# Performance work log

Measured on AMD Instinct MI355X. Metric: run time of the kernel, lower is better.

The kernel has to match this reference:

```python
import jax, jax.numpy as jnp
import numpy as np

B, F, O, DEG = 8192, 512, 512, 15  # degree+1 = 16 basis terms


def setup_inputs() -> dict:
    key = jax.random.key(0)
    k1, k2, k3 = jax.random.split(key, 3)
    x = jax.random.normal(k1, (B, F), dtype=jnp.float32)
    coeffs = jax.random.normal(k2, (F, O, DEG + 1), dtype=jnp.float32) * 0.05
    base_weight = jax.random.normal(k3, (F, O), dtype=jnp.float32) * 0.05
    return {"x": x, "coeffs": coeffs, "base_weight": base_weight}


def _chebyshev_basis(x, degree):
    # x: [B, F] -> basis: [B, F, degree+1], vectorized across all features.
    t = jnp.tanh(x)
    T0 = jnp.ones_like(t)
    T1 = t
    basis = [T0, T1]
    for _ in range(2, degree + 1):
        basis.append(2.0 * t * basis[-1] - basis[-2])
    return jnp.stack(basis, axis=-1)  # [B, F, D+1]


def reference(x, coeffs, base_weight):
    basis = _chebyshev_basis(x, DEG)                      # [B, F, D+1]
    poly_out = jnp.einsum('bin,ion->bo', basis, coeffs)   # [B, O]
    kl = jnp.zeros((1,), dtype=x.dtype)
    residual = x @ base_weight                            # [B, O]
    return (poly_out + residual, kl)
```

## Files before the change

### kernel.cpp

```cpp
#include <hip/hip_runtime.h>
#include <hip/hip_bf16.h>
#include <stdint.h>

#define MB_ 8192
#define FD  512
#define OD  512
#define KD  8704
#define KBASIS 8192
#define BT_KS   1088
#define BT_CHUNKS_PER_CT (BT_KS * 128)
#define BT_BYTES_PER_CT  (BT_CHUNKS_PER_CT * 16)
#define TOFF 98304

typedef __attribute__((ext_vector_type(4))) float f32x4;
typedef __attribute__((ext_vector_type(8))) short bf16x8;
typedef __attribute__((ext_vector_type(4))) unsigned int u32x4;
typedef __attribute__((ext_vector_type(2))) unsigned int u32x2;

__device__ __forceinline__ void gload_lds16(const void* g, void* l) {
  __builtin_amdgcn_global_load_lds((const __attribute__((address_space(1))) void*)g,
                                   (__attribute__((address_space(3))) void*)l,
                                   16, 0, 0);
}

__device__ __forceinline__ uint32_t bf_rtn(float f) {
  uint32_t u = __float_as_uint(f);
  return (u + 0x7fffu + ((u >> 16) & 1u)) >> 16;
}

__device__ __forceinline__ uint32_t pk(float a, float b) {
  uint32_t r;
  asm("v_cvt_pk_bf16_f32 %0, %1, %2" : "=v"(r) : "v"(a), "v"(b));
  return r;
}

__global__ __launch_bounds__(256) void k_tanh(const float* __restrict__ x,
                                              float* __restrict__ t,
                                              uint16_t* __restrict__ xbf) {
  int i = blockIdx.x * 256 + threadIdx.x;
  f32x4 v = ((const f32x4*)x)[i];
  f32x4 tv;
  tv[0] = tanhf(v[0]); tv[1] = tanhf(v[1]);
  tv[2] = tanhf(v[2]); tv[3] = tanhf(v[3]);
  ((f32x4*)t)[i] = tv;
  u32x2 p;
  p[0] = pk(v[0], v[1]);
  p[1] = pk(v[2], v[3]);
  ((u32x2*)xbf)[i] = p;
}

__global__ __launch_bounds__(256) void k_bt(const float* __restrict__ coeffs,
                                            const float* __restrict__ bw,
                                            uint16_t* __restrict__ bt2,
                                            float* __restrict__ out) {
  int tid = blockIdx.x * 256 + threadIdx.x;
  {
    int o = tid & 511, i = tid >> 9;
    const f32x4* src = (const f32x4*)(coeffs + (((size_t)(i * 512 + o)) << 4));
    f32x4 c0 = src[0], c1 = src[1], c2 = src[2], c3 = src[3];
    u32x4 qa, qb;
    qa[0] = pk(c0[0], c0[1]);
    qa[1] = pk(c0[2], c0[3]);
    qa[2] = pk(c1[0], c1[1]);
    qa[3] = pk(c1[2], c1[3]);
    qb[0] = pk(c2[0], c2[1]);
    qb[1] = pk(c2[2], c2[3]);
    qb[2] = pk(c3[0], c3[1]);
    qb[3] = pk(c3[2], c3[3]);
    int slo = ((i >> 2) << 3) | (i & 3);
    size_t cidx = (size_t)(o >> 7) * BT_CHUNKS_PER_CT + (size_t)slo * 128 + (o & 127);
    u32x4* base = (u32x4*)bt2;
    base[cidx]       = qa;
    base[cidx + 512] = qb;
  }
  {
    int o2 = tid >> 9, i2 = tid & 511;
    size_t cidx = (size_t)(o2 >> 7) * BT_CHUNKS_PER_CT + (size_t)(1024 + (i2 >> 3)) * 128 + (o2 & 127);
    bt2[cidx * 8 + (i2 & 7)] = (uint16_t)bf_rtn(bw[i2 * 512 + o2]);
  }
  if (tid == 0) out[(size_t)MB_ * OD] = 0.0f;
}

__global__ __launch_bounds__(512, 2) void k_gemm(const float* __restrict__ t,
                                                 const uint16_t* __restrict__ xbf,
                                                 const uint16_t* __restrict__ bt2,
                                                 float* __restrict__ out) {
  __shared__ __align__(128) char lds[110592];

  const int tid  = threadIdx.x;
  const int lane = tid & 63;
  const int wid  = tid >> 6;
  const int wr   = wid >> 1;
  const int wc   = wid & 1;
  const int l15  = lane & 15, l4 = lane >> 4;

  int bx  = blockIdx.x;
  int idx = bx >> 3;
  int rt  = (bx & 7) * 8 + (idx >> 2);
  int ct  = idx & 3;
  const int brow = rt << 7, bcol = ct << 7;

  const char* btbase = (const char*)bt2 + (size_t)ct * BT_BYTES_PER_CT;
  const int row = brow + wr * 32 + l15;
  const uint16_t* x0 = xbf + (size_t)row * FD;
  const uint16_t* x1 = x0 + (size_t)16 * FD;

  const char* bb0 = lds + l4 * 2048 + (wc * 64 + l15) * 16;
  const char* tb0 = lds + TOFF + (wr * 32 + l15) * 16 + l4 * 4;
  char* sBl = lds + tid * 16;
  char* sTl = lds + TOFF + wid * 1024 + lane * 16;

  const char* sBgBase = btbase + (size_t)tid * 16;
  const char* sTgBase = (const char*)t + (((size_t)(brow + wid * 64 + lane)) * FD) * 4;

  f32x4 acc[2][4];
#pragma unroll
  for (int m = 0; m < 2; ++m)
#pragma unroll
    for (int n = 0; n < 4; ++n) acc[m][n] = (f32x4)0.0f;

  u32x4 pf00 = {}, pf01 = {}, pf10 = {}, pf11 = {};

  auto stageB = [&](int s2, int b2) {
    const char* src = sBgBase + ((size_t)s2 << 14);
    gload_lds16(src, sBl + b2 * 16384);
    gload_lds16(src + 8192, sBl + b2 * 16384 + 8192);
  };
  auto stageT = [&](int s2, int b2) {
    if (wid < 2)
      gload_lds16(sTgBase + ((size_t)s2 << 4), sTl + b2 * 2048);
  };
  auto chains = [&](const char* tb, u32x4& af00, u32x4& af01,
                    u32x4& af10, u32x4& af11) {
#pragma unroll
    for (int m = 0; m < 2; ++m) {
      float tv = *(const float*)(tb + m * 256);
      float c2 = tv + tv;
      float T0 = 1.0f, T1 = tv;
      float T2  = __builtin_fmaf(c2, T1,  -T0);
      float T3  = __builtin_fmaf(c2, T2,  -T1);
      float T4  = __builtin_fmaf(c2, T3,  -T2);
      float T5  = __builtin_fmaf(c2, T4,  -T3);
      float T6  = __builtin_fmaf(c2, T5,  -T4);
      float T7  = __builtin_fmaf(c2, T6,  -T5);
      float T8  = __builtin_fmaf(c2, T7,  -T6);
      float T9  = __builtin_fmaf(c2, T8,  -T7);
      float T10 = __builtin_fmaf(c2, T9,  -T8);
      float T11 = __builtin_fmaf(c2, T10, -T9);
      float T12 = __builtin_fmaf(c2, T11, -T10);
      float T13 = __builtin_fmaf(c2, T12, -T11);
      float T14 = __builtin_fmaf(c2, T13, -T12);
      float T15 = __builtin_fmaf(c2, T14, -T13);
      u32x4 lo, hi;
      lo[0] = pk(T0,  T1);  lo[1] = pk(T2,  T3);
      lo[2] = pk(T4,  T5);  lo[3] = pk(T6,  T7);
      hi[0] = pk(T8,  T9);  hi[1] = pk(T10, T11);
      hi[2] = pk(T12, T13); hi[3] = pk(T14, T15);
      if (m == 0) { af00 = lo; af01 = hi; }
      else        { af10 = lo; af11 = hi; }
    }
  };
  auto mfma16 = [&](const char* bb, const u32x4& af00, const u32x4& af01,
                    const u32x4& af10, const u32x4& af11) {
    bf16x8 a00 = *(const bf16x8*)&af00;
    bf16x8 a01 = *(const bf16x8*)&af01;
    bf16x8 a10 = *(const bf16x8*)&af10;
    bf16x8 a11 = *(const bf16x8*)&af11;
#pragma unroll
    for (int n = 0; n < 4; ++n) {
      bf16x8 b0 = *(const bf16x8*)(bb + n * 256);
      bf16x8 b1 = *(const bf16x8*)(bb + 8192 + n * 256);
      acc[0][n] = __builtin_amdgcn_mfma_f32_16x16x32_bf16(a00, b0, acc[0][n], 0, 0, 0);
      acc[1][n] = __builtin_amdgcn_mfma_f32_16x16x32_bf16(a10, b0, acc[1][n], 0, 0, 0);
      acc[0][n] = __builtin_amdgcn_mfma_f32_16x16x32_bf16(a01, b1, acc[0][n], 0, 0, 0);
      acc[1][n] = __builtin_amdgcn_mfma_f32_16x16x32_bf16(a11, b1, acc[1][n], 0, 0, 0);
    }
  };
  auto fence_bar = [&]() {
    if (wid < 2) asm volatile("s_waitcnt vmcnt(6)" ::: "memory");
    else         asm volatile("s_waitcnt vmcnt(4)" ::: "memory");
    __builtin_amdgcn_s_barrier();
    asm volatile("" ::: "memory");
  };

  stageB(0, 0); stageT(0, 0);
  stageB(1, 1); stageT(1, 1);
  stageB(2, 2); stageT(2, 2);
  stageB(3, 3); stageT(3, 3);
  fence_bar();

  auto pairbody = [&](int s, int c0, int c1, int g0, int g1) {
    stageB(s + 4, g0); stageT(s + 4, g0);
    stageB(s + 5, g1); stageT(s + 5, g1);
    u32x4 af00, af01, af10, af11;
    chains(tb0 + c0 * 2048, af00, af01, af10, af11);
    __builtin_amdgcn_s_setprio(1);
    mfma16(bb0 + c0 * 16384, af00, af01, af10, af11);
    __builtin_amdgcn_s_setprio(0);
    chains(tb0 + c1 * 2048, af00, af01, af10, af11);
    __builtin_amdgcn_s_setprio(1);
    mfma16(bb0 + c1 * 16384, af00, af01, af10, af11);
    __builtin_amdgcn_s_setprio(0);
    fence_bar();
  };

  for (int s = 0; s < 120; s += 6) {
    pairbody(s,     0, 1, 4, 5);
    pairbody(s + 2, 2, 3, 0, 1);
    pairbody(s + 4, 4, 5, 2, 3);
  }
  pairbody(120, 0, 1, 4, 5);
  pairbody(122, 2, 3, 0, 1);

  for (int s = 124; s < 136; ++s) {
    u32x4 af00 = pf00, af01 = pf01, af10 = pf10, af11 = pf11;
    if (s >= 126 && s <= 133) stageB(s + 2, (s + 2) % 6);
    if (s >= 127 && s <= 134) {
      int kres = ((s + 1 - 128) << 6) + l4 * 8;
      pf00 = *(const u32x4*)(x0 + kres);
      pf01 = *(const u32x4*)(x0 + kres + 32);
      pf10 = *(const u32x4*)(x1 + kres);
      pf11 = *(const u32x4*)(x1 + kres + 32);
    }
    if (s < 128)
      chains(tb0 + (s % 6) * 2048, af00, af01, af10, af11);
    mfma16(bb0 + (s % 6) * 16384, af00, af01, af10, af11);
    __syncthreads();
  }

#pragma unroll
  for (int m = 0; m < 2; ++m)
#pragma unroll
    for (int n = 0; n < 4; ++n)
#pragma unroll
      for (int r = 0; r < 4; ++r) {
        int grow = brow + wr * 32 + m * 16 + l4 * 4 + r;
        int gcol = bcol + wc * 64 + n * 16 + l15;
        out[(size_t)grow * OD + gcol] = acc[m][n][r];
      }
}

extern "C" void kernel_launch(void* const* d_in, const int* in_sizes, int n_in,
                              void* d_out, int out_size, void* d_ws, size_t ws_size,
                              hipStream_t stream) {
  const float* x      = (const float*)d_in[0];
  const float* coeffs = (const float*)d_in[1];
  const float* bw     = (const float*)d_in[2];
  float* out = (float*)d_out;
  char* ws = (char*)d_ws;

  float*    t   = (float*)ws;
  uint16_t* xbf = (uint16_t*)(ws + (size_t)16777216);
  uint16_t* bt2 = (uint16_t*)(ws + (size_t)16777216 + 8388608);

  k_tanh<<<4096, 256, 0, stream>>>(x, t, xbf);
  k_bt<<<1024, 256, 0, stream>>>(coeffs, bw, bt2, out);
  k_gemm<<<256, 512, 0, stream>>>(t, xbf, bt2, out);
}
```

Measured before the change: 104.2 us.

## Halve GEMM column tile to 64 and double grid with smaller LDS footprint

Shrinks the output tile of the fused Chebyshev GEMM from 128x128 to 128x64, so 512 workgroups launch instead of 256. The B staging buffer halves, LDS drops to about 60KB and launch bounds target 4 blocks per CU, all meant to raise occupancy and fill the 256 CUs better. The fine-grained vmcnt fences are replaced by plain __syncthreads. In exchange, each block recomputes the Chebyshev basis chains for half as many outputs, which doubles the chain work and the T loads per unit of MFMA work. A-operand reuse also drops.

```diff
diff --git a/kernel.cpp b/kernel.cpp
--- a/kernel.cpp
+++ b/kernel.cpp
@@ -10,7 +10,7 @@
 #define BT_KS   1088
 #define BT_CHUNKS_PER_CT (BT_KS * 128)
 #define BT_BYTES_PER_CT  (BT_CHUNKS_PER_CT * 16)
-#define TOFF 98304
+#define TOFF 49152
 
 typedef __attribute__((ext_vector_type(4))) float f32x4;
 typedef __attribute__((ext_vector_type(8))) short bf16x8;
@@ -81,11 +81,11 @@
   if (tid == 0) out[(size_t)MB_ * OD] = 0.0f;
 }
 
-__global__ __launch_bounds__(512, 2) void k_gemm(const float* __restrict__ t,
+__global__ __launch_bounds__(512, 4) void k_gemm(const float* __restrict__ t,
                                                  const uint16_t* __restrict__ xbf,
                                                  const uint16_t* __restrict__ bt2,
                                                  float* __restrict__ out) {
-  __shared__ __align__(128) char lds[110592];
+  __shared__ __align__(128) char lds[61440];
 
   const int tid  = threadIdx.x;
   const int lane = tid & 63;
@@ -96,35 +96,34 @@
 
   int bx  = blockIdx.x;
   int idx = bx >> 3;
-  int rt  = (bx & 7) * 8 + (idx >> 2);
-  int ct  = idx & 3;
-  const int brow = rt << 7, bcol = ct << 7;
-
-  const char* btbase = (const char*)bt2 + (size_t)ct * BT_BYTES_PER_CT;
+  int rt  = (bx & 7) * 8 + (idx >> 3);
+  int ct  = idx & 7;
+  const int brow = rt << 7, bcol = ct << 6;
+
+  const char* btbase = (const char*)bt2 + (size_t)(ct >> 1) * BT_BYTES_PER_CT;
+  const int colOff = (ct & 1) * 1024;
   const int row = brow + wr * 32 + l15;
   const uint16_t* x0 = xbf + (size_t)row * FD;
   const uint16_t* x1 = x0 + (size_t)16 * FD;
 
-  const char* bb0 = lds + l4 * 2048 + (wc * 64 + l15) * 16;
+  const char* bb0 = lds + l4 * 1024 + (wc * 32 + l15) * 16;
   const char* tb0 = lds + TOFF + (wr * 32 + l15) * 16 + l4 * 4;
   char* sBl = lds + tid * 16;
   char* sTl = lds + TOFF + wid * 1024 + lane * 16;
 
-  const char* sBgBase = btbase + (size_t)tid * 16;
+  const char* sBgBase = btbase + (size_t)wid * 2048 + colOff + (size_t)lane * 16;
   const char* sTgBase = (const char*)t + (((size_t)(brow + wid * 64 + lane)) * FD) * 4;
 
-  f32x4 acc[2][4];
+  f32x4 acc[2][2];
 #pragma unroll
   for (int m = 0; m < 2; ++m)
 #pragma unroll
-    for (int n = 0; n < 4; ++n) acc[m][n] = (f32x4)0.0f;
+    for (int n = 0; n < 2; ++n) acc[m][n] = (f32x4)0.0f;
 
   u32x4 pf00 = {}, pf01 = {}, pf10 = {}, pf11 = {};
 
   auto stageB = [&](int s2, int b2) {
-    const char* src = sBgBase + ((size_t)s2 << 14);
-    gload_lds16(src, sBl + b2 * 16384);
-    gload_lds16(src + 8192, sBl + b2 * 16384 + 8192);
+    gload_lds16(sBgBase + ((size_t)s2 << 14), sBl + b2 * 8192);
   };
   auto stageT = [&](int s2, int b2) {
     if (wid < 2)
@@ -160,34 +159,31 @@
       else        { af10 = lo; af11 = hi; }
     }
   };
-  auto mfma16 = [&](const char* bb, const u32x4& af00, const u32x4& af01,
-                    const u32x4& af10, const u32x4& af11) {
+  auto mfma8 = [&](const char* bb, const u32x4& af00, const u32x4& af01,
+                   const u32x4& af10, const u32x4& af11) {
     bf16x8 a00 = *(const bf16x8*)&af00;
     bf16x8 a01 = *(const bf16x8*)&af01;
     bf16x8 a10 = *(const bf16x8*)&af10;
     bf16x8 a11 = *(const bf16x8*)&af11;
-#pragma unroll
-    for (int n = 0; n < 4; ++n) {
-      bf16x8 b0 = *(const bf16x8*)(bb + n * 256);
-      bf16x8 b1 = *(const bf16x8*)(bb + 8192 + n * 256);
-      acc[0][n] = __builtin_amdgcn_mfma_f32_16x16x32_bf16(a00, b0, acc[0][n], 0, 0, 0);
-      acc[1][n] = __builtin_amdgcn_mfma_f32_16x16x32_bf16(a10, b0, acc[1][n], 0, 0, 0);
-      acc[0][n] = __builtin_amdgcn_mfma_f32_16x16x32_bf16(a01, b1, acc[0][n], 0, 0, 0);
-      acc[1][n] = __builtin_amdgcn_mfma_f32_16x16x32_bf16(a11, b1, acc[1][n], 0, 0, 0);
-    }
-  };
-  auto fence_bar = [&]() {
-    if (wid < 2) asm volatile("s_waitcnt vmcnt(6)" ::: "memory");
-    else         asm volatile("s_waitcnt vmcnt(4)" ::: "memory");
-    __builtin_amdgcn_s_barrier();
-    asm volatile("" ::: "memory");
+    bf16x8 b00 = *(const bf16x8*)(bb);
+    bf16x8 b01 = *(const bf16x8*)(bb + 256);
+    bf16x8 b10 = *(const bf16x8*)(bb + 4096);
+    bf16x8 b11 = *(const bf16x8*)(bb + 4096 + 256);
+    acc[0][0] = __builtin_amdgcn_mfma_f32_16x16x32_bf16(a00, b00, acc[0][0], 0, 0, 0);
+    acc[0][1] = __builtin_amdgcn_mfma_f32_16x16x32_bf16(a00, b01, acc[0][1], 0, 0, 0);
+    acc[1][0] = __builtin_amdgcn_mfma_f32_16x16x32_bf16(a10, b00, acc[1][0], 0, 0, 0);
+    acc[1][1] = __builtin_amdgcn_mfma_f32_16x16x32_bf16(a10, b01, acc[1][1], 0, 0, 0);
+    acc[0][0] = __builtin_amdgcn_mfma_f32_16x16x32_bf16(a01, b10, acc[0][0], 0, 0, 0);
+    acc[0][1] = __builtin_amdgcn_mfma_f32_16x16x32_bf16(a01, b11, acc[0][1], 0, 0, 0);
+    acc[1][0] = __builtin_amdgcn_mfma_f32_16x16x32_bf16(a11, b10, acc[1][0], 0, 0, 0);
+    acc[1][1] = __builtin_amdgcn_mfma_f32_16x16x32_bf16(a11, b11, acc[1][1], 0, 0, 0);
   };
 
   stageB(0, 0); stageT(0, 0);
   stageB(1, 1); stageT(1, 1);
   stageB(2, 2); stageT(2, 2);
   stageB(3, 3); stageT(3, 3);
-  fence_bar();
+  __syncthreads();
 
   auto pairbody = [&](int s, int c0, int c1, int g0, int g1) {
     stageB(s + 4, g0); stageT(s + 4, g0);
@@ -195,13 +191,13 @@
     u32x4 af00, af01, af10, af11;
     chains(tb0 + c0 * 2048, af00, af01, af10, af11);
     __builtin_amdgcn_s_setprio(1);
-    mfma16(bb0 + c0 * 16384, af00, af01, af10, af11);
+    mfma8(bb0 + c0 * 8192, af00, af01, af10, af11);
     __builtin_amdgcn_s_setprio(0);
     chains(tb0 + c1 * 2048, af00, af01, af10, af11);
     __builtin_amdgcn_s_setprio(1);
-    mfma16(bb0 + c1 * 16384, af00, af01, af10, af11);
+    mfma8(bb0 + c1 * 8192, af00, af01, af10, af11);
     __builtin_amdgcn_s_setprio(0);
-    fence_bar();
+    __syncthreads();
   };
 
   for (int s = 0; s < 120; s += 6) {
@@ -224,18 +220,18 @@
     }
     if (s < 128)
       chains(tb0 + (s % 6) * 2048, af00, af01, af10, af11);
-    mfma16(bb0 + (s % 6) * 16384, af00, af01, af10, af11);
+    mfma8(bb0 + (s % 6) * 8192, af00, af01, af10, af11);
     __syncthreads();
   }
 
 #pragma unroll
   for (int m = 0; m < 2; ++m)
 #pragma unroll
-    for (int n = 0; n < 4; ++n)
+    for (int n = 0; n < 2; ++n)
 #pragma unroll
       for (int r = 0; r < 4; ++r) {
         int grow = brow + wr * 32 + m * 16 + l4 * 4 + r;
-        int gcol = bcol + wc * 64 + n * 16 + l15;
+        int gcol = bcol + wc * 32 + n * 16 + l15;
         out[(size_t)grow * OD + gcol] = acc[m][n][r];
       }
 }
@@ -255,5 +251,5 @@
 
   k_tanh<<<4096, 256, 0, stream>>>(x, t, xbf);
   k_bt<<<1024, 256, 0, stream>>>(coeffs, bw, bt2, out);
-  k_gemm<<<256, 512, 0, stream>>>(t, xbf, bt2, out);
-}
+  k_gemm<<<512, 512, 0, stream>>>(t, xbf, bt2, out);
+}
```

After: 114.7 us. 10.0% more time.

## Split GEMM K dimension across two block sets with partial-sum add kernel

Applied to the files above, without the earlier changes.

The fused Chebyshev/residual GEMM is split along K into two halves. 256 blocks handle the basis terms for the first half of the features and write to the output, while another 256 blocks handle the rest plus the residual x·W part and write to a workspace buffer. A separate kernel then adds the two partials. The LDS pipeline is cut from 6 to 4 stages to shrink shared memory for 4 blocks per CU, and stage refills are moved after a barrier. The aim is to fill more of the machine (512 blocks instead of 256), at the cost of an extra 16 MB partial write/read and another launch, with a fallback when the workspace is too small.

```diff
diff --git a/kernel.cpp b/kernel.cpp
--- a/kernel.cpp
+++ b/kernel.cpp
@@ -10,7 +10,12 @@
 #define BT_KS   1088
 #define BT_CHUNKS_PER_CT (BT_KS * 128)
 #define BT_BYTES_PER_CT  (BT_CHUNKS_PER_CT * 16)
-#define TOFF 98304
+#define TOFF 65536
+#define WS_T    16777216ull
+#define WS_XBF  8388608ull
+#define WS_BT2  8912896ull
+#define WS_P1_OFF (WS_T + WS_XBF + WS_BT2)
+#define WS_NEED   (WS_P1_OFF + 16777216ull)
 
 typedef __attribute__((ext_vector_type(4))) float f32x4;
 typedef __attribute__((ext_vector_type(8))) short bf16x8;
@@ -81,11 +86,13 @@
   if (tid == 0) out[(size_t)MB_ * OD] = 0.0f;
 }
 
-__global__ __launch_bounds__(512, 2) void k_gemm(const float* __restrict__ t,
-                                                 const uint16_t* __restrict__ xbf,
-                                                 const uint16_t* __restrict__ bt2,
-                                                 float* __restrict__ out) {
-  __shared__ __align__(128) char lds[110592];
+template <int MODE>
+__device__ __forceinline__ void gemm_body(int bx, char* lds,
+                                          const float* __restrict__ t,
+                                          const uint16_t* __restrict__ xbf,
+                                          const uint16_t* __restrict__ bt2,
+                                          float* __restrict__ outp) {
+  constexpr int S0 = (MODE == 2) ? 68 : 0;
 
   const int tid  = threadIdx.x;
   const int lane = tid & 63;
@@ -94,7 +101,6 @@
   const int wc   = wid & 1;
   const int l15  = lane & 15, l4 = lane >> 4;
 
-  int bx  = blockIdx.x;
   int idx = bx >> 3;
   int rt  = (bx & 7) * 8 + (idx >> 2);
   int ct  = idx & 3;
@@ -121,14 +127,14 @@
 
   u32x4 pf00 = {}, pf01 = {}, pf10 = {}, pf11 = {};
 
-  auto stageB = [&](int s2, int b2) {
-    const char* src = sBgBase + ((size_t)s2 << 14);
+  auto stageB = [&](int gs, int b2) {
+    const char* src = sBgBase + ((size_t)gs << 14);
     gload_lds16(src, sBl + b2 * 16384);
     gload_lds16(src + 8192, sBl + b2 * 16384 + 8192);
   };
-  auto stageT = [&](int s2, int b2) {
+  auto stageT = [&](int gs, int b2) {
     if (wid < 2)
-      gload_lds16(sTgBase + ((size_t)s2 << 4), sTl + b2 * 2048);
+      gload_lds16(sTgBase + ((size_t)gs << 4), sTl + b2 * 2048);
   };
   auto chains = [&](const char* tb, u32x4& af00, u32x4& af01,
                     u32x4& af10, u32x4& af11) {
@@ -180,18 +186,9 @@
     if (wid < 2) asm volatile("s_waitcnt vmcnt(6)" ::: "memory");
     else         asm volatile("s_waitcnt vmcnt(4)" ::: "memory");
     __builtin_amdgcn_s_barrier();
-    asm volatile("" ::: "memory");
-  };
-
-  stageB(0, 0); stageT(0, 0);
-  stageB(1, 1); stageT(1, 1);
-  stageB(2, 2); stageT(2, 2);
-  stageB(3, 3); stageT(3, 3);
-  fence_bar();
-
-  auto pairbody = [&](int s, int c0, int c1, int g0, int g1) {
-    stageB(s + 4, g0); stageT(s + 4, g0);
-    stageB(s + 5, g1); stageT(s + 5, g1);
+    __builtin_amdgcn_sched_barrier(0);
+  };
+  auto pairbody = [&](int s, int c0, int c1) {
     u32x4 af00, af01, af10, af11;
     chains(tb0 + c0 * 2048, af00, af01, af10, af11);
     __builtin_amdgcn_s_setprio(1);
@@ -201,31 +198,60 @@
     __builtin_amdgcn_s_setprio(1);
     mfma16(bb0 + c1 * 16384, af00, af01, af10, af11);
     __builtin_amdgcn_s_setprio(0);
+    __builtin_amdgcn_s_barrier();
+    __builtin_amdgcn_sched_barrier(0);
+    stageB(S0 + s + 4, c0); stageT(S0 + s + 4, c0);
+    stageB(S0 + s + 5, c1); stageT(S0 + s + 5, c1);
     fence_bar();
   };
 
-  for (int s = 0; s < 120; s += 6) {
-    pairbody(s,     0, 1, 4, 5);
-    pairbody(s + 2, 2, 3, 0, 1);
-    pairbody(s + 4, 4, 5, 2, 3);
-  }
-  pairbody(120, 0, 1, 4, 5);
-  pairbody(122, 2, 3, 0, 1);
-
-  for (int s = 124; s < 136; ++s) {
-    u32x4 af00 = pf00, af01 = pf01, af10 = pf10, af11 = pf11;
-    if (s >= 126 && s <= 133) stageB(s + 2, (s + 2) % 6);
-    if (s >= 127 && s <= 134) {
-      int kres = ((s + 1 - 128) << 6) + l4 * 8;
-      pf00 = *(const u32x4*)(x0 + kres);
-      pf01 = *(const u32x4*)(x0 + kres + 32);
-      pf10 = *(const u32x4*)(x1 + kres);
-      pf11 = *(const u32x4*)(x1 + kres + 32);
-    }
-    if (s < 128)
-      chains(tb0 + (s % 6) * 2048, af00, af01, af10, af11);
-    mfma16(bb0 + (s % 6) * 16384, af00, af01, af10, af11);
-    __syncthreads();
+  stageB(S0 + 0, 0); stageT(S0 + 0, 0);
+  stageB(S0 + 1, 1); stageT(S0 + 1, 1);
+  stageB(S0 + 2, 2); stageT(S0 + 2, 2);
+  stageB(S0 + 3, 3); stageT(S0 + 3, 3);
+  fence_bar();
+
+  if constexpr (MODE == 0) {
+    for (int s = 0; s < 120; s += 4) { pairbody(s, 0, 1); pairbody(s + 2, 2, 3); }
+    pairbody(120, 0, 1); pairbody(122, 2, 3);
+    for (int s = 124; s < 136; ++s) {
+      u32x4 af00 = pf00, af01 = pf01, af10 = pf10, af11 = pf11;
+      if (s >= 126 && s <= 133) stageB(s + 2, (s + 2) & 3);
+      if (s >= 127 && s <= 134) {
+        int kres = ((s + 1 - 128) << 6) + l4 * 8;
+        pf00 = *(const u32x4*)(x0 + kres);
+        pf01 = *(const u32x4*)(x0 + kres + 32);
+        pf10 = *(const u32x4*)(x1 + kres);
+        pf11 = *(const u32x4*)(x1 + kres + 32);
+      }
+      if (s < 128) chains(tb0 + (s & 3) * 2048, af00, af01, af10, af11);
+      mfma16(bb0 + (s & 3) * 16384, af00, af01, af10, af11);
+      __syncthreads();
+    }
+  } else if constexpr (MODE == 1) {
+    for (int s = 0; s < 64; s += 4) { pairbody(s, 0, 1); pairbody(s + 2, 2, 3); }
+    for (int s = 64; s < 68; ++s) {
+      u32x4 af00, af01, af10, af11;
+      chains(tb0 + (s & 3) * 2048, af00, af01, af10, af11);
+      mfma16(bb0 + (s & 3) * 16384, af00, af01, af10, af11);
+      __syncthreads();
+    }
+  } else {
+    for (int s = 0; s < 56; s += 4) { pairbody(s, 0, 1); pairbody(s + 2, 2, 3); }
+    for (int s = 56; s < 68; ++s) {
+      u32x4 af00 = pf00, af01 = pf01, af10 = pf10, af11 = pf11;
+      if (s >= 58 && s <= 65) stageB(68 + s + 2, (s + 2) & 3);
+      if (s >= 59 && s <= 66) {
+        int kres = ((s + 1 - 60) << 6) + l4 * 8;
+        pf00 = *(const u32x4*)(x0 + kres);
+        pf01 = *(const u32x4*)(x0 + kres + 32);
+        pf10 = *(const u32x4*)(x1 + kres);
+        pf11 = *(const u32x4*)(x1 + kres + 32);
+      }
+      if (s < 60) chains(tb0 + (s & 3) * 2048, af00, af01, af10, af11);
+      mfma16(bb0 + (s & 3) * 16384, af00, af01, af10, af11);
+      __syncthreads();
+    }
   }
 
 #pragma unroll
@@ -236,8 +262,35 @@
       for (int r = 0; r < 4; ++r) {
         int grow = brow + wr * 32 + m * 16 + l4 * 4 + r;
         int gcol = bcol + wc * 64 + n * 16 + l15;
-        out[(size_t)grow * OD + gcol] = acc[m][n][r];
+        outp[(size_t)grow * OD + gcol] = acc[m][n][r];
       }
+}
+
+__global__ __launch_bounds__(512, 4) void k_gemm_split(const float* __restrict__ t,
+                                                       const uint16_t* __restrict__ xbf,
+                                                       const uint16_t* __restrict__ bt2,
+                                                       float* __restrict__ out,
+                                                       float* __restrict__ p1) {
+  __shared__ __align__(128) char lds[73728];
+  if (blockIdx.x < 256) gemm_body<1>(blockIdx.x,       lds, t, xbf, bt2, out);
+  else                  gemm_body<2>(blockIdx.x - 256, lds, t, xbf, bt2, p1);
+}
+
+__global__ __launch_bounds__(512, 2) void k_gemm_full(const float* __restrict__ t,
+                                                      const uint16_t* __restrict__ xbf,
+                                                      const uint16_t* __restrict__ bt2,
+                                                      float* __restrict__ out) {
+  __shared__ __align__(128) char lds[73728];
+  gemm_body<0>(blockIdx.x, lds, t, xbf, bt2, out);
+}
+
+__global__ __launch_bounds__(256) void k_add(float* __restrict__ out,
+                                             const float* __restrict__ p1) {
+  size_t i = (size_t)blockIdx.x * 256 + threadIdx.x;
+  f32x4 a = ((const f32x4*)out)[i];
+  f32x4 b = ((const f32x4*)p1)[i];
+  a[0] += b[0]; a[1] += b[1]; a[2] += b[2]; a[3] += b[3];
+  ((f32x4*)out)[i] = a;
 }
 
 extern "C" void kernel_launch(void* const* d_in, const int* in_sizes, int n_in,
@@ -250,10 +303,16 @@
   char* ws = (char*)d_ws;
 
   float*    t   = (float*)ws;
-  uint16_t* xbf = (uint16_t*)(ws + (size_t)16777216);
-  uint16_t* bt2 = (uint16_t*)(ws + (size_t)16777216 + 8388608);
+  uint16_t* xbf = (uint16_t*)(ws + WS_T);
+  uint16_t* bt2 = (uint16_t*)(ws + WS_T + WS_XBF);
+  float*    p1  = (float*)(ws + WS_P1_OFF);
 
   k_tanh<<<4096, 256, 0, stream>>>(x, t, xbf);
   k_bt<<<1024, 256, 0, stream>>>(coeffs, bw, bt2, out);
-  k_gemm<<<256, 512, 0, stream>>>(t, xbf, bt2, out);
-}
+  if (ws_size >= WS_NEED) {
+    k_gemm_split<<<512, 512, 0, stream>>>(t, xbf, bt2, out, p1);
+    k_add<<<4096, 256, 0, stream>>>(out, p1);
+  } else {
+    k_gemm_full<<<256, 512, 0, stream>>>(t, xbf, bt2, out);
+  }
+}
```

Measured after the change: 104.2 us. About the same (+0.0%).
